# Kernel tuning notes

Hardware: AMD Instinct MI355X
Metric: run time of the kernel (lower is better)

Reference implementation:

```python
import jax, jax.numpy as jnp
import numpy as np

B, N, NPOINT = 4, 8192, 1024
RADII = (0.1, 0.2, 0.4)
NSAMPLES = (16, 32, 128)
MLPS = ((16, 16, 32), (32, 32, 64), (32, 48, 64))  # divide_ratio = 2 -> 32+64+64 = 160 channels


def setup_inputs():
    key = jax.random.key(0)
    ks = jax.random.split(key, 24)
    inp = {"pcd": jax.random.uniform(ks[0], (B, N, 3), jnp.float32)}
    ki = 1
    for bi, mlp in enumerate(MLPS):
        cin = 3
        for li, cout in enumerate(mlp):
            inp[f"w{bi}_{li}"] = jax.random.normal(ks[ki], (cin, cout), jnp.float32) / np.float32(np.sqrt(cin))
            inp[f"b{bi}_{li}"] = jnp.zeros((cout,), jnp.float32)
            ki += 1
            cin = cout
    inp["w_out"] = jax.random.normal(ks[ki], (160, 1), jnp.float32) / np.float32(np.sqrt(160.0))
    inp["b_out"] = jnp.zeros((1,), jnp.float32)
    inp["divide_ratio"] = 2
    return inp


def _fps(xyz, npoint):
    # Farthest point sampling: sequential argmax over running min-distance.
    b, n, _ = xyz.shape
    d0 = jnp.full((b, n), 1e10, xyz.dtype)
    f0 = jnp.zeros((b,), jnp.int32)

    def step(carry, _):
        dist, far = carry
        c = jnp.take_along_axis(xyz, far[:, None, None], axis=1)  # [B,1,3]
        dist = jnp.minimum(dist, jnp.sum((xyz - c) ** 2, -1))
        return (dist, jnp.argmax(dist, -1).astype(jnp.int32)), far

    _, idx = jax.lax.scan(step, (d0, f0), None, length=npoint)
    return idx.T  # [B, npoint]


def _ball_query(sqrdist, radius, nsample):
    # For each center take first nsample points within radius; pad with first hit.
    n = sqrdist.shape[-1]
    ar = jnp.arange(n, dtype=jnp.int32)
    idx = jnp.where(sqrdist <= radius * radius, ar[None, None, :], n)
    idx = jnp.sort(idx, axis=-1)[..., :nsample]
    first = idx[..., :1]
    return jnp.where(idx == n, first, idx)  # [B,S,nsample]


def _forward(pcd, layers, w_out, b_out):
    fps_idx = _fps(pcd, NPOINT)
    new_xyz = jnp.take_along_axis(pcd, fps_idx[..., None], axis=1)  # [B,S,3]
    # pairwise squared distance, computed once and reused for all radii  [B,S,N]
    sqrdist = (jnp.sum(new_xyz ** 2, -1)[:, :, None]
               + jnp.sum(pcd ** 2, -1)[:, None, :]
               - 2.0 * jnp.einsum("bsd,bnd->bsn", new_xyz, pcd))
    feats = []
    for radius, nsample, lw in zip(RADII, NSAMPLES, layers):
        idx = _ball_query(sqrdist, radius, nsample)
        grouped = jnp.take_along_axis(pcd[:, None, :, :], idx[..., None], axis=2)  # [B,S,ns,3]
        h = grouped - new_xyz[:, :, None, :]  # centered local coords (l0_points is None)
        for w, b in lw:
            h = jax.nn.relu(h @ w + b)  # 1x1 conv == dense over last dim
        feats.append(jnp.max(h, axis=2))  # max-pool over neighbors -> [B,S,C]
    f = jnp.concatenate(feats, axis=-1)  # [B,S,160]
    return f @ w_out + b_out  # Conv1d(160,1,k=1) -> [B,S,1]


def reference(pcd, w0_0, b0_0, w0_1, b0_1, w0_2, b0_2,
              w1_0, b1_0, w1_1, b1_1, w1_2, b1_2,
              w2_0, b2_0, w2_1, b2_1, w2_2, b2_2,
              w_out, b_out, divide_ratio):
    del divide_ratio  # fixed to 2 by construction (conv1 expects 160 channels)
    layers = (((w0_0, b0_0), (w0_1, b0_1), (w0_2, b0_2)),
              ((w1_0, b1_0), (w1_1, b1_1), (w1_2, b1_2)),
              ((w2_0, b2_0), (w2_1, b2_1), (w2_2, b2_2)))
    return _forward(pcd, layers, w_out, b_out)
```

## Files before the change

### kernel.cpp

```cpp
#include <hip/hip_runtime.h>

#define BB 4
#define NN 8192
#define SS 1024

static __device__ __forceinline__ float sq3(float x, float y, float z) {
  return __fadd_rn(__fadd_rn(__fmul_rn(x, x), __fmul_rn(y, y)), __fmul_rn(z, z));
}

__global__ void prep_kernel(const float* __restrict__ pcd,
                            float* __restrict__ xs, float* __restrict__ ys,
                            float* __restrict__ zs, float* __restrict__ sp) {
  int i = blockIdx.x * 256 + threadIdx.x;
  if (i < BB * NN) {
    float x = pcd[3 * i], y = pcd[3 * i + 1], z = pcd[3 * i + 2];
    xs[i] = x; ys[i] = y; zs[i] = z;
    sp[i] = sq3(x, y, z);
  }
}

__global__ __launch_bounds__(256) void fps_kernel(const float* __restrict__ xs,
                                                  const float* __restrict__ ys,
                                                  const float* __restrict__ zs,
                                                  float* __restrict__ new_xyz,
                                                  float* __restrict__ s_new) {
  const int b = blockIdx.x;
  const float* X = xs + b * NN;
  const float* Y = ys + b * NN;
  const float* Z = zs + b * NN;
  __shared__ unsigned long long wkey[2][4];

  const int tid = threadIdx.x;
  float lx[32], ly[32], lz[32], dst[32];
#pragma unroll
  for (int k = 0; k < 32; ++k) {
    int i = tid + (k << 8);
    lx[k] = X[i]; ly[k] = Y[i]; lz[k] = Z[i];
    dst[k] = 1e10f;
  }
  float cx = X[0], cy = Y[0], cz = Z[0];

  for (int t = 0; t < SS; ++t) {
    if (tid == 0) {
      float* nx = new_xyz + 3 * (b * SS + t);
      nx[0] = cx; nx[1] = cy; nx[2] = cz;
      s_new[b * SS + t] = sq3(cx, cy, cz);
    }
    float lmax = -1.0f;
    int lidx = 0;
#pragma unroll
    for (int k = 0; k < 32; ++k) {
      float dx = __fsub_rn(lx[k], cx);
      float dy = __fsub_rn(ly[k], cy);
      float dz = __fsub_rn(lz[k], cz);
      float d = __fadd_rn(__fadd_rn(__fmul_rn(dx, dx), __fmul_rn(dy, dy)),
                          __fmul_rn(dz, dz));
      d = fminf(dst[k], d);
      dst[k] = d;
      if (d > lmax) { lmax = d; lidx = tid + (k << 8); }
    }
    unsigned long long key =
        ((unsigned long long)__float_as_uint(lmax) << 32) |
        (unsigned)(8191 - lidx);
#pragma unroll
    for (int off = 32; off > 0; off >>= 1) {
      unsigned long long o = __shfl_xor(key, off, 64);
      key = o > key ? o : key;
    }
    if ((tid & 63) == 0) wkey[t & 1][tid >> 6] = key;
    __syncthreads();
    unsigned long long k0 = wkey[t & 1][0], k1 = wkey[t & 1][1];
    unsigned long long k2 = wkey[t & 1][2], k3 = wkey[t & 1][3];
    k0 = k1 > k0 ? k1 : k0;
    k2 = k3 > k2 ? k3 : k2;
    k0 = k2 > k0 ? k2 : k0;
    int gi = 8191 - (int)(k0 & 8191ull);
    int gis = __builtin_amdgcn_readfirstlane(gi);
    cx = X[gis]; cy = Y[gis]; cz = Z[gis];
  }
}

struct KCParams {
  const float* xs; const float* ys; const float* zs; const float* sp;
  const float* new_xyz; const float* s_new;
  const float* wA[3]; const float* bA[3];
  const float* wB[3]; const float* bB[3];
  const float* wC[3]; const float* bC[3];
  const float* w_out; const float* b_out;
  float* out;
};

template <int NS, int C1, int C2, int C3>
__device__ __forceinline__ void run_branch(
    int tid, int off, int fbase,
    const float* __restrict__ xs, const float* __restrict__ ys,
    const float* __restrict__ zs, float cx, float cy, float cz,
    const float* __restrict__ wA, const float* __restrict__ bA,
    const float* __restrict__ wB, const float* __restrict__ bB,
    const float* __restrict__ wC, const float* __restrict__ bC,
    const int* sidx, float (*g)[4], float (*h1)[36], float (*h2)[52],
    float (*redm)[64], float* feats) {
  if (tid < NS) {
    int ip = sidx[off + tid];
    g[tid][0] = xs[ip] - cx;
    g[tid][1] = ys[ip] - cy;
    g[tid][2] = zs[ip] - cz;
  }
  __syncthreads();
  {
    const int cc = tid % C1, sg = tid / C1;
    const int G = 128 / C1;
    float wx = wA[cc], wy = wA[C1 + cc], wz = wA[2 * C1 + cc], bb = bA[cc];
    for (int s0 = sg; s0 < NS; s0 += G) {
      float acc = fmaf(g[s0][0], wx, fmaf(g[s0][1], wy, fmaf(g[s0][2], wz, bb)));
      h1[s0][cc] = fmaxf(acc, 0.0f);
    }
  }
  __syncthreads();
  {
    const int G = 128 / C2;
    if (tid < G * C2) {
      const int cc = tid % C2, sg = tid / C2;
      float wr[C1];
#pragma unroll
      for (int k = 0; k < C1; ++k) wr[k] = wB[k * C2 + cc];
      float bb = bB[cc];
#pragma unroll 2
      for (int s0 = sg; s0 < NS; s0 += G) {
        const float4* hr = (const float4*)(&h1[s0][0]);
        float acc = bb;
#pragma unroll
        for (int k4 = 0; k4 < C1 / 4; ++k4) {
          float4 hv = hr[k4];
          acc = fmaf(hv.x, wr[4 * k4 + 0], acc);
          acc = fmaf(hv.y, wr[4 * k4 + 1], acc);
          acc = fmaf(hv.z, wr[4 * k4 + 2], acc);
          acc = fmaf(hv.w, wr[4 * k4 + 3], acc);
        }
        h2[s0][cc] = fmaxf(acc, 0.0f);
      }
    }
  }
  __syncthreads();
  {
    const int G = 128 / C3;
    const int cc = tid % C3, sg = tid / C3;
    float wr[C2];
#pragma unroll
    for (int k = 0; k < C2; ++k) wr[k] = wC[k * C3 + cc];
    float bb = bC[cc];
    float pm = -1e30f;
#pragma unroll 2
    for (int s0 = sg; s0 < NS; s0 += G) {
      const float4* hr = (const float4*)(&h2[s0][0]);
      float acc = bb;
#pragma unroll
      for (int k4 = 0; k4 < C2 / 4; ++k4) {
        float4 hv = hr[k4];
        acc = fmaf(hv.x, wr[4 * k4 + 0], acc);
        acc = fmaf(hv.y, wr[4 * k4 + 1], acc);
        acc = fmaf(hv.z, wr[4 * k4 + 2], acc);
        acc = fmaf(hv.w, wr[4 * k4 + 3], acc);
      }
      pm = fmaxf(pm, fmaxf(acc, 0.0f));
    }
    redm[sg][cc] = pm;
  }
  __syncthreads();
  if (tid < C3) {
    float m = redm[0][tid];
#pragma unroll
    for (int gg = 1; gg < 128 / C3; ++gg) m = fmaxf(m, redm[gg][tid]);
    feats[fbase + tid] = m;
  }
  __syncthreads();
}

__global__ __launch_bounds__(128) void sa_kernel(KCParams p) {
  const int bid = blockIdx.x;
  const int b = bid >> 10;
  const int tid = threadIdx.x;
  const int lane = tid & 63;
  const int wv = tid >> 6;

  __shared__ __align__(16) float g[128][4];
  __shared__ __align__(16) float h1s[128][36];
  __shared__ __align__(16) float h2s[128][52];
  __shared__ int sidx[176];
  __shared__ int lid0[2][16];
  __shared__ int lid1[2][32];
  __shared__ int lid2[2][128];
  __shared__ int scnt[2][3];
  __shared__ float feats[160];
  __shared__ __align__(16) float redm[4][64];
  __shared__ float rsum[2];

  const float* xs = p.xs + b * NN;
  const float* ys = p.ys + b * NN;
  const float* zs = p.zs + b * NN;
  const float* sp = p.sp + b * NN;
  const float cx = p.new_xyz[3 * bid];
  const float cy = p.new_xyz[3 * bid + 1];
  const float cz = p.new_xyz[3 * bid + 2];
  const float snew = p.s_new[bid];

  {
    const float R2_0 = (float)(0.1 * 0.1);
    const float R2_1 = (float)(0.2 * 0.2);
    const float R2_2 = (float)(0.4 * 0.4);
    const unsigned long long below = (1ull << lane) - 1ull;
    int c0 = 0, c1 = 0, c2 = 0;
    int pt = wv * 4096 + lane;
    float x = xs[pt], y = ys[pt], z = zs[pt], s2v = sp[pt];
    for (int it = 0; it < 64; ++it) {
      float xx = x, yy = y, zz = z, ss = s2v;
      if (it < 63) {
        int q = pt + 64;
        x = xs[q]; y = ys[q]; z = zs[q]; s2v = sp[q];
      }
      float dt = fmaf(zz, cz, fmaf(yy, cy, __fmul_rn(xx, cx)));
      float d = __fsub_rn(__fadd_rn(snew, ss), __fmul_rn(2.0f, dt));
      bool m2 = d <= R2_2;
      unsigned long long bm = __ballot(m2);
      if (m2) { int r = c2 + __popcll(bm & below); if (r < 128) lid2[wv][r] = pt; }
      c2 += __popcll(bm);
      bool m1 = d <= R2_1;
      bm = __ballot(m1);
      if (m1) { int r = c1 + __popcll(bm & below); if (r < 32) lid1[wv][r] = pt; }
      c1 += __popcll(bm);
      bool m0 = d <= R2_0;
      bm = __ballot(m0);
      if (m0) { int r = c0 + __popcll(bm & below); if (r < 16) lid0[wv][r] = pt; }
      c0 += __popcll(bm);
      pt += 64;
      if (c0 >= 16 && c1 >= 32 && c2 >= 128) break;
    }
    if (lane == 0) {
      scnt[wv][0] = c0 < 16 ? c0 : 16;
      scnt[wv][1] = c1 < 32 ? c1 : 32;
      scnt[wv][2] = c2 < 128 ? c2 : 128;
    }
  }
  __syncthreads();
  {
    int a0 = scnt[0][0], a1 = scnt[0][1], a2 = scnt[0][2];
    int b0 = scnt[1][0], b1 = scnt[1][1], b2 = scnt[1][2];
    int n0 = min(a0 + b0, 16), n1 = min(a1 + b1, 32), n2 = min(a2 + b2, 128);
    int f0 = a0 ? lid0[0][0] : lid0[1][0];
    int f1 = a1 ? lid1[0][0] : lid1[1][0];
    int f2 = a2 ? lid2[0][0] : lid2[1][0];
    for (int j = tid; j < 176; j += 128) {
      int v;
      if (j < 16) {
        int sl = j;
        v = sl < a0 ? lid0[0][sl] : (sl < n0 ? lid0[1][sl - a0] : f0);
      } else if (j < 48) {
        int sl = j - 16;
        v = sl < a1 ? lid1[0][sl] : (sl < n1 ? lid1[1][sl - a1] : f1);
      } else {
        int sl = j - 48;
        v = sl < a2 ? lid2[0][sl] : (sl < n2 ? lid2[1][sl - a2] : f2);
      }
      sidx[j] = v;
    }
  }
  __syncthreads();

  run_branch<16, 16, 16, 32>(tid, 0, 0, xs, ys, zs, cx, cy, cz,
                             p.wA[0], p.bA[0], p.wB[0], p.bB[0], p.wC[0], p.bC[0],
                             sidx, g, h1s, h2s, redm, feats);
  run_branch<32, 32, 32, 64>(tid, 16, 32, xs, ys, zs, cx, cy, cz,
                             p.wA[1], p.bA[1], p.wB[1], p.bB[1], p.wC[1], p.bC[1],
                             sidx, g, h1s, h2s, redm, feats);
  run_branch<128, 32, 48, 64>(tid, 48, 96, xs, ys, zs, cx, cy, cz,
                              p.wA[2], p.bA[2], p.wB[2], p.bB[2], p.wC[2], p.bC[2],
                              sidx, g, h1s, h2s, redm, feats);

  float part = feats[tid] * p.w_out[tid];
  if (tid < 32) part += feats[128 + tid] * p.w_out[128 + tid];
#pragma unroll
  for (int off = 32; off > 0; off >>= 1) part += __shfl_xor(part, off, 64);
  if (lane == 0) rsum[wv] = part;
  __syncthreads();
  if (tid == 0) p.out[bid] = rsum[0] + rsum[1] + p.b_out[0];
}

extern "C" void kernel_launch(void* const* d_in, const int* in_sizes, int n_in,
                              void* d_out, int out_size, void* d_ws, size_t ws_size,
                              hipStream_t stream) {
  const float* pcd = (const float*)d_in[0];
  float* ws = (float*)d_ws;
  float* xs = ws;
  float* ys = xs + BB * NN;
  float* zs = ys + BB * NN;
  float* sp = zs + BB * NN;
  float* new_xyz = sp + BB * NN;
  float* s_new = new_xyz + BB * SS * 3;

  prep_kernel<<<(BB * NN + 255) / 256, 256, 0, stream>>>(pcd, xs, ys, zs, sp);
  fps_kernel<<<BB, 256, 0, stream>>>(xs, ys, zs, new_xyz, s_new);

  KCParams p;
  p.xs = xs; p.ys = ys; p.zs = zs; p.sp = sp;
  p.new_xyz = new_xyz; p.s_new = s_new;
  for (int br = 0; br < 3; ++br) {
    p.wA[br] = (const float*)d_in[1 + 6 * br + 0];
    p.bA[br] = (const float*)d_in[1 + 6 * br + 1];
    p.wB[br] = (const float*)d_in[1 + 6 * br + 2];
    p.bB[br] = (const float*)d_in[1 + 6 * br + 3];
    p.wC[br] = (const float*)d_in[1 + 6 * br + 4];
    p.bC[br] = (const float*)d_in[1 + 6 * br + 5];
  }
  p.w_out = (const float*)d_in[19];
  p.b_out = (const float*)d_in[20];
  p.out = (float*)d_out;

  sa_kernel<<<BB * SS, 128, 0, stream>>>(p);
}
```

Measured before the change: 1.518 ms.

## Evaluate grouped MLP per-thread in registers with LDS-staged weights

Replaces the channel-parallel shared-memory MLP (with h1/h2 tiles in LDS and many barriers) with a per-neighbor-per-thread evaluation: each thread keeps its point's activations in registers and reads weights broadcast from LDS, then max-pools with wavefront shuffles. Weights for the large branch are staged into LDS first, then the two smaller branches run concurrently on separate wavefronts. This removes most barriers and LDS activation traffic but increases register pressure and duplicates lanes for the 16/32-sample branches, which waste half or more of their wavefront.

After: 2.708 ms. 78.4% more time.

```diff
diff --git a/kernel.cpp b/kernel.cpp
--- a/kernel.cpp
+++ b/kernel.cpp
@@ -90,109 +90,94 @@
   float* out;
 };
 
-template <int NS, int C1, int C2, int C3>
-__device__ __forceinline__ void run_branch(
-    int tid, int off, int fbase,
-    const float* __restrict__ xs, const float* __restrict__ ys,
-    const float* __restrict__ zs, float cx, float cy, float cz,
-    const float* __restrict__ wA, const float* __restrict__ bA,
-    const float* __restrict__ wB, const float* __restrict__ bB,
-    const float* __restrict__ wC, const float* __restrict__ bC,
-    const int* sidx, float (*g)[4], float (*h1)[36], float (*h2)[52],
-    float (*redm)[64], float* feats) {
-  if (tid < NS) {
-    int ip = sidx[off + tid];
-    g[tid][0] = xs[ip] - cx;
-    g[tid][1] = ys[ip] - cy;
-    g[tid][2] = zs[ip] - cz;
-  }
-  __syncthreads();
+template <int C1, int C2, int C3, bool TWOWAVE>
+__device__ __forceinline__ void branch_eval(
+    const float* wb, float gx, float gy, float gz, int lane, int wv,
+    float (*redm)[64], float* feats, int fbase) {
+  const float* wA = wb;
+  const float* bA = wb + 3 * C1;
+  const float* wB = wb + 4 * C1;
+  const float* bB = wB + C1 * C2;
+  const float* wC = bB + C2;
+  const float* bC = wC + C2 * C3;
+
+  float h1[C1];
+#pragma unroll
+  for (int j = 0; j < C1; ++j) {
+    float acc = fmaf(gx, wA[j], fmaf(gy, wA[C1 + j], fmaf(gz, wA[2 * C1 + j], bA[j])));
+    h1[j] = fmaxf(acc, 0.0f);
+  }
+
+  float h2[C2];
   {
-    const int cc = tid % C1, sg = tid / C1;
-    const int G = 128 / C1;
-    float wx = wA[cc], wy = wA[C1 + cc], wz = wA[2 * C1 + cc], bb = bA[cc];
-    for (int s0 = sg; s0 < NS; s0 += G) {
-      float acc = fmaf(g[s0][0], wx, fmaf(g[s0][1], wy, fmaf(g[s0][2], wz, bb)));
-      h1[s0][cc] = fmaxf(acc, 0.0f);
-    }
-  }
-  __syncthreads();
+    const float4* wB4 = (const float4*)wB;
+    const float4* bB4 = (const float4*)bB;
+#pragma unroll
+    for (int j4 = 0; j4 < C2 / 4; ++j4) {
+      float4 acc = bB4[j4];
+#pragma unroll
+      for (int k = 0; k < C1; ++k) {
+        float4 w = wB4[k * (C2 / 4) + j4];
+        acc.x = fmaf(h1[k], w.x, acc.x);
+        acc.y = fmaf(h1[k], w.y, acc.y);
+        acc.z = fmaf(h1[k], w.z, acc.z);
+        acc.w = fmaf(h1[k], w.w, acc.w);
+      }
+      h2[4 * j4 + 0] = fmaxf(acc.x, 0.0f);
+      h2[4 * j4 + 1] = fmaxf(acc.y, 0.0f);
+      h2[4 * j4 + 2] = fmaxf(acc.z, 0.0f);
+      h2[4 * j4 + 3] = fmaxf(acc.w, 0.0f);
+    }
+  }
+
   {
-    const int G = 128 / C2;
-    if (tid < G * C2) {
-      const int cc = tid % C2, sg = tid / C2;
-      float wr[C1];
-#pragma unroll
-      for (int k = 0; k < C1; ++k) wr[k] = wB[k * C2 + cc];
-      float bb = bB[cc];
-#pragma unroll 2
-      for (int s0 = sg; s0 < NS; s0 += G) {
-        const float4* hr = (const float4*)(&h1[s0][0]);
-        float acc = bb;
-#pragma unroll
-        for (int k4 = 0; k4 < C1 / 4; ++k4) {
-          float4 hv = hr[k4];
-          acc = fmaf(hv.x, wr[4 * k4 + 0], acc);
-          acc = fmaf(hv.y, wr[4 * k4 + 1], acc);
-          acc = fmaf(hv.z, wr[4 * k4 + 2], acc);
-          acc = fmaf(hv.w, wr[4 * k4 + 3], acc);
+    const float4* wC4 = (const float4*)wC;
+    const float4* bC4 = (const float4*)bC;
+    for (int c4 = 0; c4 < C3 / 4; ++c4) {
+      float4 acc = bC4[c4];
+#pragma unroll
+      for (int k = 0; k < C2; ++k) {
+        float4 w = wC4[k * (C3 / 4) + c4];
+        acc.x = fmaf(h2[k], w.x, acc.x);
+        acc.y = fmaf(h2[k], w.y, acc.y);
+        acc.z = fmaf(h2[k], w.z, acc.z);
+        acc.w = fmaf(h2[k], w.w, acc.w);
+      }
+      float vals[4];
+      vals[0] = fmaxf(acc.x, 0.0f);
+      vals[1] = fmaxf(acc.y, 0.0f);
+      vals[2] = fmaxf(acc.z, 0.0f);
+      vals[3] = fmaxf(acc.w, 0.0f);
+#pragma unroll
+      for (int q = 0; q < 4; ++q) {
+        float r = vals[q];
+#pragma unroll
+        for (int off = 32; off > 0; off >>= 1)
+          r = fmaxf(r, __shfl_xor(r, off, 64));
+        if (lane == 0) {
+          if (TWOWAVE) redm[wv][4 * c4 + q] = r;
+          else feats[fbase + 4 * c4 + q] = r;
         }
-        h2[s0][cc] = fmaxf(acc, 0.0f);
-      }
-    }
-  }
-  __syncthreads();
-  {
-    const int G = 128 / C3;
-    const int cc = tid % C3, sg = tid / C3;
-    float wr[C2];
-#pragma unroll
-    for (int k = 0; k < C2; ++k) wr[k] = wC[k * C3 + cc];
-    float bb = bC[cc];
-    float pm = -1e30f;
-#pragma unroll 2
-    for (int s0 = sg; s0 < NS; s0 += G) {
-      const float4* hr = (const float4*)(&h2[s0][0]);
-      float acc = bb;
-#pragma unroll
-      for (int k4 = 0; k4 < C2 / 4; ++k4) {
-        float4 hv = hr[k4];
-        acc = fmaf(hv.x, wr[4 * k4 + 0], acc);
-        acc = fmaf(hv.y, wr[4 * k4 + 1], acc);
-        acc = fmaf(hv.z, wr[4 * k4 + 2], acc);
-        acc = fmaf(hv.w, wr[4 * k4 + 3], acc);
-      }
-      pm = fmaxf(pm, fmaxf(acc, 0.0f));
-    }
-    redm[sg][cc] = pm;
-  }
-  __syncthreads();
-  if (tid < C3) {
-    float m = redm[0][tid];
-#pragma unroll
-    for (int gg = 1; gg < 128 / C3; ++gg) m = fmaxf(m, redm[gg][tid]);
-    feats[fbase + tid] = m;
-  }
-  __syncthreads();
-}
-
-__global__ __launch_bounds__(128) void sa_kernel(KCParams p) {
+      }
+    }
+  }
+}
+
+__global__ __launch_bounds__(128, 3) void sa_kernel(KCParams p) {
   const int bid = blockIdx.x;
   const int b = bid >> 10;
   const int tid = threadIdx.x;
   const int lane = tid & 63;
   const int wv = tid >> 6;
 
-  __shared__ __align__(16) float g[128][4];
-  __shared__ __align__(16) float h1s[128][36];
-  __shared__ __align__(16) float h2s[128][52];
+  __shared__ __align__(16) float wbuf[4848];
   __shared__ int sidx[176];
   __shared__ int lid0[2][16];
   __shared__ int lid1[2][32];
   __shared__ int lid2[2][128];
   __shared__ int scnt[2][3];
   __shared__ float feats[160];
-  __shared__ __align__(16) float redm[4][64];
+  __shared__ float redm[2][64];
   __shared__ float rsum[2];
 
   const float* xs = p.xs + b * NN;
@@ -242,6 +227,11 @@
     }
   }
   __syncthreads();
+
+  auto stage = [&](int off, const float* src, int n) {
+    for (int i = tid; i < n; i += 128) wbuf[off + i] = src[i];
+  };
+
   {
     int a0 = scnt[0][0], a1 = scnt[0][1], a2 = scnt[0][2];
     int b0 = scnt[1][0], b1 = scnt[1][1], b2 = scnt[1][2];
@@ -263,18 +253,48 @@
       }
       sidx[j] = v;
     }
-  }
-  __syncthreads();
-
-  run_branch<16, 16, 16, 32>(tid, 0, 0, xs, ys, zs, cx, cy, cz,
-                             p.wA[0], p.bA[0], p.wB[0], p.bB[0], p.wC[0], p.bC[0],
-                             sidx, g, h1s, h2s, redm, feats);
-  run_branch<32, 32, 32, 64>(tid, 16, 32, xs, ys, zs, cx, cy, cz,
-                             p.wA[1], p.bA[1], p.wB[1], p.bB[1], p.wC[1], p.bC[1],
-                             sidx, g, h1s, h2s, redm, feats);
-  run_branch<128, 32, 48, 64>(tid, 48, 96, xs, ys, zs, cx, cy, cz,
-                              p.wA[2], p.bA[2], p.wB[2], p.bB[2], p.wC[2], p.bC[2],
-                              sidx, g, h1s, h2s, redm, feats);
+    stage(0, p.wA[2], 96);
+    stage(96, p.bA[2], 32);
+    stage(128, p.wB[2], 1536);
+    stage(1664, p.bB[2], 48);
+    stage(1712, p.wC[2], 3072);
+    stage(4784, p.bC[2], 64);
+  }
+  __syncthreads();
+
+  int i3 = sidx[48 + tid];
+  float g3x = xs[i3] - cx, g3y = ys[i3] - cy, g3z = zs[i3] - cz;
+  float g2x, g2y, g2z;
+  if (wv == 0) {
+    int i2 = sidx[16 + (lane & 31)];
+    g2x = xs[i2] - cx; g2y = ys[i2] - cy; g2z = zs[i2] - cz;
+  } else {
+    int i1 = sidx[lane & 15];
+    g2x = xs[i1] - cx; g2y = ys[i1] - cy; g2z = zs[i1] - cz;
+  }
+
+  branch_eval<32, 48, 64, true>(wbuf, g3x, g3y, g3z, lane, wv, redm, feats, 96);
+  __syncthreads();
+  if (tid < 64) feats[96 + tid] = fmaxf(redm[0][tid], redm[1][tid]);
+  stage(0, p.wA[1], 96);
+  stage(96, p.bA[1], 32);
+  stage(128, p.wB[1], 1024);
+  stage(1152, p.bB[1], 32);
+  stage(1184, p.wC[1], 2048);
+  stage(3232, p.bC[1], 64);
+  stage(3296, p.wA[0], 48);
+  stage(3344, p.bA[0], 16);
+  stage(3360, p.wB[0], 256);
+  stage(3616, p.bB[0], 16);
+  stage(3632, p.wC[0], 512);
+  stage(4144, p.bC[0], 32);
+  __syncthreads();
+
+  if (wv == 0)
+    branch_eval<32, 32, 64, false>(wbuf, g2x, g2y, g2z, lane, 0, redm, feats, 32);
+  else
+    branch_eval<16, 16, 32, false>(wbuf + 3296, g2x, g2y, g2z, lane, 1, redm, feats, 0);
+  __syncthreads();
 
   float part = feats[tid] * p.w_out[tid];
   if (tid < 32) part += feats[128 + tid] * p.w_out[128 + tid];
```
